# Optimization experiments

Hardware: AMD Instinct MI355X
Metric: run time of the kernel (lower is better)

## Reference

```python
import jax, jax.numpy as jnp
import numpy as np
from jax import lax

N, D, E = 20000, 1024, 320000
H, DH, M, ITERS, KC = 8, 64, 256, 6, 33   # nystrom heads, head dim, landmarks, pinv iters, res conv kernel
WQK, WATT, NC = 256, 128, 2               # custom-attn dim, MIL attn dim, n_classes


def _pinv(x, iters):
    # Moore-Penrose iterative pseudo-inverse (lucidrains nystrom-attention)
    ax = jnp.abs(x)
    z = jnp.swapaxes(x, -1, -2) / (ax.sum(-1).max() * ax.sum(-2).max())
    I = jnp.eye(x.shape[-1], dtype=x.dtype)
    for _ in range(iters):
        xz = x @ z
        z = 0.25 * z @ (13. * I - xz @ (15. * I - xz @ (7. * I - xz)))
    return z


def _nystrom(x, qkv_w, out_w, out_b, res_w):
    b, n, d = x.shape
    pad = (M - n % M) % M
    xp = jnp.pad(x, ((0, 0), (pad, 0), (0, 0)))  # pad at front, as in torch impl
    npd = n + pad
    q, k, v = jnp.split(xp @ qkv_w, 3, axis=-1)
    heads = lambda t: t.reshape(b, npd, H, DH).transpose(0, 2, 1, 3)  # [b,h,n,dh]
    q = heads(q) * (DH ** -0.5); k = heads(k); v = heads(v)
    l = npd // M
    ql = q.reshape(b, H, M, l, DH).sum(3) / l   # landmark means
    kl = k.reshape(b, H, M, l, DH).sum(3) / l
    a1 = jax.nn.softmax(jnp.einsum('bhid,bhjd->bhij', q, kl), -1)   # [b,h,n,m]
    a2 = jax.nn.softmax(jnp.einsum('bhid,bhjd->bhij', ql, kl), -1)  # [b,h,m,m]
    a3 = jax.nn.softmax(jnp.einsum('bhid,bhjd->bhij', ql, k), -1)   # [b,h,m,n]
    out = (a1 @ _pinv(a2, ITERS)) @ (a3 @ v)
    # depthwise residual conv along the sequence dim, per head
    res = lax.conv_general_dilated(v, res_w, (1, 1), ((KC // 2, KC // 2), (0, 0)),
                                   dimension_numbers=('NCHW', 'OIHW', 'NCHW'),
                                   feature_group_count=H)
    out = (out + res).transpose(0, 2, 1, 3).reshape(b, npd, H * DH)
    return (out @ out_w + out_b)[:, -n:]


def _forward(bag, adj_vals, qkv_w, out_w, out_b, res_w, wq_w, wq_b, wk_w, wk_b,
             wv_w, wv_b, va_w, va_b, ua_w, ua_b, wa_w, wa_b, fc_w, fc_b, fc_b2,
             adj_rows, adj_cols):
    enc = _nystrom(bag, qkv_w, out_w, out_b, res_w)        # [1,N,D]
    encoder_output = enc[0] + bag                           # xg + dense -> [1,N,D]
    # CustomAttention: per-edge q.k over sparse adjacency indices
    q = encoder_output[0] @ wq_w + wq_b                     # [N,256]
    k = encoder_output[0] @ wk_w + wk_b
    e = jnp.sum(q[adj_rows] * k[adj_cols], -1) / (WQK ** 0.5)
    # NeighborAggregator: sparse elementwise mul with adj then row-sum
    A_raw = jax.ops.segment_sum(e * adj_vals, adj_rows, num_segments=N)
    alpha = jax.nn.softmax(A_raw)                           # [N]
    value = bag @ wv_w + wv_b                               # [1,N,D]
    xl = alpha[:, None] * value                             # [1,N,D]
    sw = jax.nn.sigmoid(-xl) ** 2
    xo = xl * 2. * sw + 2. * encoder_output * (1. - sw)     # [1,N,D]
    # gated MIL attention (softmax over dim 0 of [1,N,1], as in source)
    inst = jnp.tanh(xo @ va_w + va_b) * jax.nn.sigmoid(xo @ ua_w + ua_b)
    k_alpha = jax.nn.softmax(inst @ wa_w + wa_b, axis=0)    # [1,N,1]
    pooled = (k_alpha * xo)[0].mean(0, keepdims=True)       # mean pooling -> [1,D]
    out = pooled @ fc_w + fc_b + fc_b2                      # [1,NC]
    return out, A_raw, k_alpha


def setup_inputs() -> dict:
    key = jax.random.key(0)
    ks = jax.random.split(key, 20)
    s = 0.02
    p = lambda k, shape: jax.random.normal(k, shape, jnp.float32) * s
    z = lambda n: jnp.zeros((n,), jnp.float32)
    return {
        'bag': jax.random.normal(ks[0], (1, N, D), jnp.float32),
        'adj_vals': jnp.ones((E,), jnp.float32),
        'qkv_w': p(ks[1], (D, 3 * H * DH)),
        'out_w': p(ks[2], (H * DH, D)), 'out_b': z(D),
        'res_w': p(ks[3], (H, 1, KC, 1)),
        'wq_w': p(ks[4], (D, WQK)), 'wq_b': z(WQK),
        'wk_w': p(ks[5], (D, WQK)), 'wk_b': z(WQK),
        'wv_w': p(ks[6], (D, D)), 'wv_b': z(D),
        'va_w': p(ks[7], (D, WATT)), 'va_b': z(WATT),
        'ua_w': p(ks[8], (D, WATT)), 'ua_b': z(WATT),
        'wa_w': p(ks[9], (WATT, 1)), 'wa_b': z(1),
        'fc_w': p(ks[10], (D, NC)), 'fc_b': z(NC), 'fc_b2': z(NC),
        'adj_rows': jax.random.randint(ks[11], (E,), 0, N),
        'adj_cols': jax.random.randint(ks[12], (E,), 0, N),
    }


def reference(bag, adj_vals, qkv_w, out_w, out_b, res_w, wq_w, wq_b, wk_w, wk_b,
              wv_w, wv_b, va_w, va_b, ua_w, ua_b, wa_w, wa_b, fc_w, fc_b, fc_b2,
              adj_rows, adj_cols):
    return _forward(bag, adj_vals, qkv_w, out_w, out_b, res_w, wq_w, wq_b, wk_w, wk_b,
                    wv_w, wv_b, va_w, va_b, ua_w, ua_b, wa_w, wa_b, fc_w, fc_b, fc_b2,
                    adj_rows, adj_cols)
```

## Files before the change

### kernel.cpp

```cpp
#include <hip/hip_runtime.h>
#include <math.h>

constexpr int NTOK = 20000;
constexpr int DIM  = 1024;
constexpr int NEDGE= 320000;
constexpr int NH   = 8;
constexpr int DH   = 64;
constexpr int NLM  = 256;
constexpr int PADF = 224;
constexpr int NPD  = 20224;
constexpr int LGRP = 79;
constexpr int PITERS = 6;
constexpr int JSPL = 16;
constexpr int JLEN = NPD / JSPL;
constexpr int NCHK = 79;

typedef unsigned short u16;
typedef _Float16 f16x8 __attribute__((ext_vector_type(8)));
typedef float    f32x4 __attribute__((ext_vector_type(4)));
typedef u16      u16x8 __attribute__((ext_vector_type(8)));
typedef u16      u16x4 __attribute__((ext_vector_type(4)));

__device__ __forceinline__ float warpSum(float v){
  #pragma unroll
  for (int o = 32; o; o >>= 1) v += __shfl_xor(v, o);
  return v;
}
__device__ __forceinline__ float warpMax(float v){
  #pragma unroll
  for (int o = 32; o; o >>= 1) v = fmaxf(v, __shfl_xor(v, o));
  return v;
}
__device__ __forceinline__ u16 f2h(float x){
  _Float16 h = (_Float16)x; return __builtin_bit_cast(u16, h);
}
__device__ __forceinline__ float h2f(u16 u){
  return (float)__builtin_bit_cast(_Float16, u);
}
__device__ __forceinline__ int swz3(int r){ return (r ^ (r >> 2)) & 3; }

__global__ void zero_kernel(float* __restrict__ p, int n)
{
  int i = blockIdx.x * 256 + threadIdx.x;
  if (i < n) p[i] = 0.f;
}

__global__ __launch_bounds__(256) void tsplit_kernel(
    const float* __restrict__ W, u16* __restrict__ Th, u16* __restrict__ Tl,
    int Kd, int Nd)
{
  __shared__ float tile[32][33];
  const int t = threadIdx.x, bx = blockIdx.x, by = blockIdx.y;
  {
    int kk = t >> 3, n4 = (t & 7) * 4;
    float4 v = *(const float4*)&W[(size_t)(by*32 + kk) * Nd + bx*32 + n4];
    tile[kk][n4+0] = v.x; tile[kk][n4+1] = v.y;
    tile[kk][n4+2] = v.z; tile[kk][n4+3] = v.w;
  }
  __syncthreads();
  int nn = t >> 3, k4 = (t & 7) * 4;
  u16x4 hv, lv;
  #pragma unroll
  for (int c = 0; c < 4; ++c) {
    float x = tile[k4 + c][nn];
    u16 h = f2h(x);
    hv[c] = h;
    lv[c] = f2h(x - h2f(h));
  }
  size_t o = (size_t)(bx*32 + nn) * Kd + by*32 + k4;
  *(u16x4*)&Th[o] = hv;
  *(u16x4*)&Tl[o] = lv;
}

__global__ __launch_bounds__(256) void gemm_h2_kernel(
    const float* __restrict__ A, int ashift, int arows,
    const u16* __restrict__ BTh, const u16* __restrict__ BTl,
    const float* __restrict__ bias, const float* __restrict__ add,
    float* __restrict__ C,
    float* __restrict__ Qd, float* __restrict__ Kd2, float* __restrict__ Vd,
    int M, int N, int Kdim)
{
  __shared__ __align__(16) u16 AsH[128*32];
  __shared__ __align__(16) u16 AsL[128*32];
  __shared__ __align__(16) u16 BsH[128*32];
  __shared__ __align__(16) u16 BsL[128*32];
  const int tid = threadIdx.x, lane = tid & 63, wv = tid >> 6;
  const int wr = wv >> 1, wc = wv & 1;
  const int bm = blockIdx.y * 128, bn = blockIdx.x * 128;

  const int rowA = tid >> 1, half = tid & 1;
  const int rg = bm + rowA;
  const unsigned r_a = (unsigned)(rg - ashift);
  const bool av = r_a < (unsigned)arows;
  const float* Ap = A + (size_t)r_a * Kdim + half * 16;
  const u16* Bph = BTh + (size_t)(bn + rowA) * Kdim + half * 16;
  const u16* Bpl = BTl + (size_t)(bn + rowA) * Kdim + half * 16;
  const int swa = swz3(rowA);
  const int pg0 = (half*2) ^ swa, pg1 = (half*2 + 1) ^ swa;
  u16* wA_h0 = &AsH[rowA*32 + pg0*8]; u16* wA_h1 = &AsH[rowA*32 + pg1*8];
  u16* wA_l0 = &AsL[rowA*32 + pg0*8]; u16* wA_l1 = &AsL[rowA*32 + pg1*8];
  u16* wB_h0 = &BsH[rowA*32 + pg0*8]; u16* wB_h1 = &BsH[rowA*32 + pg1*8];
  u16* wB_l0 = &BsL[rowA*32 + pg0*8]; u16* wB_l1 = &BsL[rowA*32 + pg1*8];

  f32x4 acc[4][4];
  #pragma unroll
  for (int i = 0; i < 4; ++i)
    #pragma unroll
    for (int j = 0; j < 4; ++j) acc[i][j] = 0;

  const int lg = lane >> 4;
  const int l15 = lane & 15;

  for (int kt = 0; kt < Kdim; kt += 32) {
    float x[16];
    if (av) {
      float4 v0 = *(const float4*)(Ap + kt);
      float4 v1 = *(const float4*)(Ap + kt + 4);
      float4 v2 = *(const float4*)(Ap + kt + 8);
      float4 v3 = *(const float4*)(Ap + kt + 12);
      x[0]=v0.x; x[1]=v0.y; x[2]=v0.z; x[3]=v0.w;
      x[4]=v1.x; x[5]=v1.y; x[6]=v1.z; x[7]=v1.w;
      x[8]=v2.x; x[9]=v2.y; x[10]=v2.z; x[11]=v2.w;
      x[12]=v3.x; x[13]=v3.y; x[14]=v3.z; x[15]=v3.w;
    } else {
      #pragma unroll
      for (int e = 0; e < 16; ++e) x[e] = 0.f;
    }
    u16x8 ah0, ah1, al0, al1;
    #pragma unroll
    for (int e = 0; e < 8; ++e) {
      u16 h = f2h(x[e]);      ah0[e] = h; al0[e] = f2h(x[e]     - h2f(h));
      u16 h2 = f2h(x[8+e]);   ah1[e] = h2; al1[e] = f2h(x[8+e] - h2f(h2));
    }
    u16x8 bh0 = *(const u16x8*)(Bph + kt);
    u16x8 bh1 = *(const u16x8*)(Bph + kt + 8);
    u16x8 bl0 = *(const u16x8*)(Bpl + kt);
    u16x8 bl1 = *(const u16x8*)(Bpl + kt + 8);

    __syncthreads();
    *(u16x8*)wA_h0 = ah0; *(u16x8*)wA_h1 = ah1;
    *(u16x8*)wA_l0 = al0; *(u16x8*)wA_l1 = al1;
    *(u16x8*)wB_h0 = bh0; *(u16x8*)wB_h1 = bh1;
    *(u16x8*)wB_l0 = bl0; *(u16x8*)wB_l1 = bl1;
    __syncthreads();

    f16x8 bh[4], bl[4];
    #pragma unroll
    for (int j = 0; j < 4; ++j) {
      int lb = wc*64 + j*16 + l15;
      int offb = lb*32 + ((lg ^ swz3(lb)) * 8);
      bh[j] = __builtin_bit_cast(f16x8, *(const u16x8*)&BsH[offb]);
      bl[j] = __builtin_bit_cast(f16x8, *(const u16x8*)&BsL[offb]);
    }
    #pragma unroll
    for (int i = 0; i < 4; ++i) {
      int la = wr*64 + i*16 + l15;
      int offa = la*32 + ((lg ^ swz3(la)) * 8);
      f16x8 ah = __builtin_bit_cast(f16x8, *(const u16x8*)&AsH[offa]);
      f16x8 al = __builtin_bit_cast(f16x8, *(const u16x8*)&AsL[offa]);
      #pragma unroll
      for (int j = 0; j < 4; ++j) {
        acc[i][j] = __builtin_amdgcn_mfma_f32_16x16x32_f16(ah, bh[j], acc[i][j], 0, 0, 0);
        acc[i][j] = __builtin_amdgcn_mfma_f32_16x16x32_f16(ah, bl[j], acc[i][j], 0, 0, 0);
        acc[i][j] = __builtin_amdgcn_mfma_f32_16x16x32_f16(al, bh[j], acc[i][j], 0, 0, 0);
      }
    }
  }

  if (Qd) {
    #pragma unroll
    for (int i = 0; i < 4; ++i) {
      int row0 = bm + wr*64 + i*16 + (lane>>4)*4;
      #pragma unroll
      for (int j = 0; j < 4; ++j) {
        int col = bn + wc*64 + j*16 + l15;
        int which = col >> 9;
        float* dst = (which == 0) ? Qd : (which == 1) ? Kd2 : Vd;
        float sc = (which == 0) ? 0.125f : 1.f;
        int h = (col >> 6) & 7, dh = col & 63;
        #pragma unroll
        for (int r = 0; r < 4; ++r) {
          int gr = row0 + r;
          dst[((size_t)h * NPD + gr) * 64 + dh] = acc[i][j][r] * sc;
        }
      }
    }
  } else {
    #pragma unroll
    for (int i = 0; i < 4; ++i) {
      int row0 = bm + wr*64 + i*16 + (lane>>4)*4;
      #pragma unroll
      for (int j = 0; j < 4; ++j) {
        int col = bn + wc*64 + j*16 + l15;
        float bv = bias ? bias[col] : 0.f;
        #pragma unroll
        for (int r = 0; r < 4; ++r) {
          int gr = row0 + r;
          if (gr < M) {
            float v = acc[i][j][r] + bv;
            if (add) v += add[(size_t)gr * N + col];
            C[(size_t)gr * N + col] = v;
          }
        }
      }
    }
  }
}

__global__ __launch_bounds__(256) void bgemm64_kernel(
    const float* __restrict__ A, const float* __restrict__ B, float* __restrict__ C,
    int Msub, int Nsub, int Ksub, float dval, int useDiag, float scale)
{
  const int h = blockIdx.z;
  const float* Ah = A + (size_t)h * Msub * Ksub;
  const float* Bh = B + (size_t)h * Ksub * Nsub;
  float* Ch = C + (size_t)h * Msub * Nsub;
  __shared__ float As[16][68];
  __shared__ float Bs[16][64];
  const int tid = threadIdx.x, tx = tid & 15, ty = tid >> 4;
  const int bm = blockIdx.y * 64, bn = blockIdx.x * 64;
  float acc[4][4] = {};
  for (int k0 = 0; k0 < Ksub; k0 += 16) {
    float ra[4], rb[4];
    #pragma unroll
    for (int i = 0; i < 4; ++i) {
      int e = tid + 256 * i;
      ra[i] = Ah[(size_t)(bm + (e >> 4)) * Ksub + k0 + (e & 15)];
      int brow = k0 + (e >> 6), bcol = bn + (e & 63);
      float bv = Bh[(size_t)brow * Nsub + bcol];
      if (useDiag) bv = ((brow == bcol) ? dval : 0.f) - bv;
      rb[i] = bv;
    }
    __syncthreads();
    #pragma unroll
    for (int i = 0; i < 4; ++i) {
      int e = tid + 256 * i;
      As[e & 15][e >> 4] = ra[i];
      Bs[e >> 6][e & 63] = rb[i];
    }
    __syncthreads();
    #pragma unroll
    for (int k = 0; k < 16; ++k) {
      float4 a = *(const float4*)&As[k][ty*4];
      float4 b = *(const float4*)&Bs[k][tx*4];
      float avv[4] = {a.x,a.y,a.z,a.w};
      float bvv[4] = {b.x,b.y,b.z,b.w};
      #pragma unroll
      for (int i = 0; i < 4; ++i)
        #pragma unroll
        for (int j = 0; j < 4; ++j)
          acc[i][j] += avv[i] * bvv[j];
    }
    __syncthreads();
  }
  #pragma unroll
  for (int i = 0; i < 4; ++i) {
    float4 v = {acc[i][0]*scale, acc[i][1]*scale, acc[i][2]*scale, acc[i][3]*scale};
    *(float4*)&Ch[(size_t)(bm + ty*4 + i) * Nsub + bn + tx*4] = v;
  }
}

__global__ __launch_bounds__(64) void landmark_kernel(
    const float* __restrict__ src, float* __restrict__ dst)
{
  int m = blockIdx.x, h = blockIdx.y, d = threadIdx.x;
  const float* p = src + ((size_t)h * NPD + (size_t)m * LGRP) * 64 + d;
  float acc = 0.f;
  for (int j = 0; j < LGRP; ++j) acc += p[(size_t)j * 64];
  dst[((size_t)h * NLM + m) * 64 + d] = acc / (float)LGRP;
}

__global__ __launch_bounds__(256) void a2_kernel(
    const float* __restrict__ qlm, const float* __restrict__ klm, float* __restrict__ a2)
{
  int i = blockIdx.x, h = blockIdx.y, t = threadIdx.x;
  int w = t >> 6, lane = t & 63;
  __shared__ float qs[64];
  __shared__ float wr[4], wr2[4];
  if (t < 64) qs[t] = qlm[((size_t)h * NLM + i) * 64 + t];
  __syncthreads();
  const float* kr = klm + ((size_t)h * NLM + t) * 64;
  float s = 0.f;
  #pragma unroll
  for (int d2 = 0; d2 < 64; d2 += 4) {
    float4 kv = *(const float4*)(kr + d2);
    s += qs[d2]*kv.x + qs[d2+1]*kv.y + qs[d2+2]*kv.z + qs[d2+3]*kv.w;
  }
  float mx = warpMax(s);
  if (lane == 0) wr[w] = mx;
  __syncthreads();
  mx = fmaxf(fmaxf(wr[0], wr[1]), fmaxf(wr[2], wr[3]));
  float e = expf(s - mx);
  float sm = warpSum(e);
  if (lane == 0) wr2[w] = sm;
  __syncthreads();
  sm = wr2[0] + wr2[1] + wr2[2] + wr2[3];
  a2[((size_t)h * NLM + i) * NLM + t] = e / sm;
}

__global__ __launch_bounds__(256) void rowcolmax_kernel(
    const float* __restrict__ a2, float* __restrict__ scal)
{
  int h = blockIdx.x >> 1, mode = blockIdx.x & 1, t = threadIdx.x;
  int w = t >> 6, lane = t & 63;
  float sum = 0.f;
  if (mode == 0) {
    const float* p = a2 + ((size_t)h * NLM + t) * NLM;
    for (int j = 0; j < NLM; ++j) sum += p[j];
  } else {
    const float* p = a2 + (size_t)h * NLM * NLM + t;
    for (int i = 0; i < NLM; ++i) sum += p[(size_t)i * NLM];
  }
  float mx = warpMax(sum);
  __shared__ float wr[4];
  if (lane == 0) wr[w] = mx;
  __syncthreads();
  if (t == 0) {
    float m2 = fmaxf(fmaxf(wr[0], wr[1]), fmaxf(wr[2], wr[3]));
    atomicMax((int*)&scal[mode], __float_as_int(m2));
  }
}

__global__ __launch_bounds__(256) void initz_kernel(
    const float* __restrict__ a2, const float* __restrict__ scal, float* __restrict__ z)
{
  int i = blockIdx.x, h = blockIdx.y, t = threadIdx.x;
  float inv = 1.f / (scal[0] * scal[1]);
  z[((size_t)h * NLM + i) * NLM + t] = a2[((size_t)h * NLM + t) * NLM + i] * inv;
}

__global__ __launch_bounds__(256) void st_gemm_kernel(
    const float* __restrict__ K, const float* __restrict__ QLM,
    float* __restrict__ ST, int hbase)
{
  const int z = blockIdx.z, h = hbase + z;
  const float* A  = K   + (size_t)h * NPD * 64;
  const float* Bq = QLM + (size_t)h * NLM * 64;
  float* C = ST + (size_t)z * NPD * NLM;
  __shared__ float As[16][132];
  __shared__ float Bs[16][132];
  const int tid = threadIdx.x;
  const int tx = tid & 15, ty = tid >> 4;
  const int bm = blockIdx.y * 128, bn = blockIdx.x * 128;
  float acc[8][8] = {};
  for (int k0 = 0; k0 < 64; k0 += 16) {
    float ra[8], rb[8];
    #pragma unroll
    for (int i = 0; i < 8; ++i) {
      int e = tid + 256 * i;
      ra[i] = A[(size_t)(bm + (e >> 4)) * 64 + k0 + (e & 15)];
      rb[i] = Bq[(size_t)(bn + (e & 127)) * 64 + k0 + (e >> 7)];
    }
    __syncthreads();
    #pragma unroll
    for (int i = 0; i < 8; ++i) {
      int e = tid + 256 * i;
      As[e & 15][e >> 4]  = ra[i];
      Bs[e >> 7][e & 127] = rb[i];
    }
    __syncthreads();
    #pragma unroll
    for (int k = 0; k < 16; ++k) {
      float4 a0 = *(const float4*)&As[k][ty*4];
      float4 a1 = *(const float4*)&As[k][64 + ty*4];
      float4 b0 = *(const float4*)&Bs[k][tx*4];
      float4 b1 = *(const float4*)&Bs[k][64 + tx*4];
      float av[8] = {a0.x,a0.y,a0.z,a0.w,a1.x,a1.y,a1.z,a1.w};
      float bv[8] = {b0.x,b0.y,b0.z,b0.w,b1.x,b1.y,b1.z,b1.w};
      #pragma unroll
      for (int i = 0; i < 8; ++i)
        #pragma unroll
        for (int j = 0; j < 8; ++j)
          acc[i][j] += av[i] * bv[j];
    }
  }
  #pragma unroll
  for (int i = 0; i < 8; ++i) {
    int r = bm + ((i < 4) ? (ty*4 + i) : (64 + ty*4 + (i - 4)));
    #pragma unroll
    for (int jh = 0; jh < 2; ++jh) {
      int c0 = bn + jh*64 + tx*4;
      float4 v = {acc[i][jh*4+0], acc[i][jh*4+1], acc[i][jh*4+2], acc[i][jh*4+3]};
      *(float4*)&C[(size_t)r * NLM + c0] = v;
    }
  }
}

__global__ __launch_bounds__(256) void smax1_kernel(
    const float* __restrict__ ST, float* __restrict__ PMAX)
{
  int c = blockIdx.x, z = blockIdx.y, i = threadIdx.x;
  const float* p = ST + (size_t)z * NPD * NLM + (size_t)c * 256 * NLM + i;
  float mx = -INFINITY;
  #pragma unroll 8
  for (int jj = 0; jj < 256; ++jj) mx = fmaxf(mx, p[(size_t)jj * NLM]);
  PMAX[((size_t)z * NCHK + c) * NLM + i] = mx;
}

__global__ __launch_bounds__(256) void smax2_kernel(
    const float* __restrict__ PMAX, float* __restrict__ MXB, int hbase)
{
  int z = blockIdx.x, i = threadIdx.x;
  float mx = -INFINITY;
  for (int c = 0; c < NCHK; ++c)
    mx = fmaxf(mx, PMAX[((size_t)z * NCHK + c) * NLM + i]);
  MXB[(size_t)(hbase + z) * NLM + i] = mx;
}

__global__ __launch_bounds__(256) void pv_kernel(
    const float* __restrict__ ST, const float* __restrict__ V,
    const float* __restrict__ MXB, float* __restrict__ AVACC,
    float* __restrict__ LSACC, int hbase)
{
  const int z = blockIdx.z, h = hbase + z;
  const int i0 = blockIdx.y * 64;
  const int j0 = blockIdx.x * JLEN;
  const float* STh = ST + (size_t)z * NPD * NLM;
  const float* Vh  = V  + (size_t)h * NPD * 64;
  const int tid = threadIdx.x, tx = tid & 15, ty = tid >> 4;
  const int il = tid & 63;
  const float mloc = MXB[(size_t)h * NLM + i0 + il];
  __shared__ float As[16][68];
  __shared__ float Bs[16][64];
  __shared__ float S4[4][64];
  float acc[4][4] = {};
  float psum = 0.f;
  for (int k0 = 0; k0 < JLEN; k0 += 16) {
    float pa[4], pb[4];
    #pragma unroll
    for (int r = 0; r < 4; ++r) {
      int jj = (tid >> 6) + 4 * r;
      int j  = j0 + k0 + jj;
      pa[r] = expf(STh[(size_t)j * NLM + i0 + il] - mloc);
      pb[r] = Vh[(size_t)j * 64 + il];
      psum += pa[r];
    }
    __syncthreads();
    #pragma unroll
    for (int r = 0; r < 4; ++r) {
      int jj = (tid >> 6) + 4 * r;
      As[jj][il] = pa[r];
      Bs[jj][il] = pb[r];
    }
    __syncthreads();
    #pragma unroll
    for (int k = 0; k < 16; ++k) {
      float4 a = *(const float4*)&As[k][ty*4];
      float4 b = *(const float4*)&Bs[k][tx*4];
      float av[4] = {a.x,a.y,a.z,a.w};
      float bv[4] = {b.x,b.y,b.z,b.w};
      #pragma unroll
      for (int i = 0; i < 4; ++i)
        #pragma unroll
        for (int j = 0; j < 4; ++j)
          acc[i][j] += av[i] * bv[j];
    }
    __syncthreads();
  }
  S4[tid >> 6][il] = psum;
  __syncthreads();
  if (tid < 64)
    atomicAdd(&LSACC[(size_t)h * NLM + i0 + tid],
              S4[0][tid] + S4[1][tid] + S4[2][tid] + S4[3][tid]);
  #pragma unroll
  for (int i = 0; i < 4; ++i)
    #pragma unroll
    for (int d = 0; d < 4; ++d)
      atomicAdd(&AVACC[((size_t)h * NLM + i0 + ty*4 + i) * 64 + tx*4 + d], acc[i][d]);
}

__global__ __launch_bounds__(64) void avnorm_kernel(
    const float* __restrict__ AVACC, const float* __restrict__ LSACC,
    float* __restrict__ AV)
{
  int m = blockIdx.x, h = blockIdx.y, d = threadIdx.x;
  size_t idx = ((size_t)h * NLM + m) * 64 + d;
  AV[idx] = AVACC[idx] / LSACC[(size_t)h * NLM + m];
}

__global__ __launch_bounds__(256) void a1_fused_kernel(
    const float* __restrict__ Q, const float* __restrict__ klm,
    const float* __restrict__ W, float* __restrict__ O1)
{
  int h = blockIdx.y;
  int rb = blockIdx.x * 8;
  int t = threadIdx.x;
  int w = t >> 6, lane = t & 63;
  __shared__ float qs[8][64];
  __shared__ float ps[8][256];
  __shared__ float Wl[128 * 64];
  for (int e = t; e < 8 * 64; e += 256) {
    int r = e >> 6, d2 = e & 63;
    qs[r][d2] = Q[((size_t)h * NPD + PADF + rb + r) * 64 + d2];
  }
  __syncthreads();
  const float* kr = klm + ((size_t)h * NLM + t) * 64;
  float s[8] = {};
  #pragma unroll
  for (int d2 = 0; d2 < 64; d2 += 4) {
    float4 kv = *(const float4*)(kr + d2);
    #pragma unroll
    for (int r = 0; r < 8; ++r)
      s[r] += qs[r][d2]*kv.x + qs[r][d2+1]*kv.y + qs[r][d2+2]*kv.z + qs[r][d2+3]*kv.w;
  }
  #pragma unroll
  for (int r = 0; r < 8; ++r) ps[r][t] = s[r];
  __syncthreads();
  for (int r = w; r < 8; r += 4) {
    float v0 = ps[r][lane], v1 = ps[r][lane+64], v2 = ps[r][lane+128], v3 = ps[r][lane+192];
    float mx = warpMax(fmaxf(fmaxf(v0, v1), fmaxf(v2, v3)));
    float e0 = expf(v0-mx), e1 = expf(v1-mx), e2 = expf(v2-mx), e3 = expf(v3-mx);
    float inv = 1.f / warpSum(e0 + e1 + e2 + e3);
    ps[r][lane] = e0*inv; ps[r][lane+64] = e1*inv; ps[r][lane+128] = e2*inv; ps[r][lane+192] = e3*inv;
  }
  const float* Wh = W + (size_t)h * NLM * 64;
  int r0 = t >> 6, d = t & 63;
  float accA = 0.f, accB = 0.f;
  for (int half = 0; half < 2; ++half) {
    __syncthreads();
    for (int e = t; e < 2048; e += 256)
      ((float4*)Wl)[e] = ((const float4*)(Wh + (size_t)half * 8192))[e];
    __syncthreads();
    #pragma unroll 16
    for (int j = 0; j < 128; ++j) {
      float wv = Wl[j * 64 + d];
      accA += ps[r0][half*128 + j] * wv;
      accB += ps[r0 + 4][half*128 + j] * wv;
    }
  }
  O1[((size_t)rb + r0) * 512 + h*64 + d] = accA;
  O1[((size_t)rb + r0 + 4) * 512 + h*64 + d] = accB;
}

__global__ __launch_bounds__(512) void conv_res_kernel(
    const float* __restrict__ V, const float* __restrict__ rw, float* __restrict__ O1)
{
  int t = threadIdx.x;
  int h = t >> 6, d = t & 63;
  int i = PADF + blockIdx.x;
  __shared__ float wsm[264];
  if (t < 264) wsm[t] = rw[t];
  __syncthreads();
  const float* vp = V + ((size_t)h * NPD + i - 16) * 64 + d;
  float acc = 0.f;
  #pragma unroll
  for (int k = 0; k < 33; ++k) {
    int row = i - 16 + k;
    float vv = (row < NPD) ? vp[(size_t)k * 64] : 0.f;
    acc += wsm[h*33 + k] * vv;
  }
  O1[(size_t)blockIdx.x * 512 + t] += acc;
}

__global__ __launch_bounds__(256) void edge_kernel(
    const float* __restrict__ Q2, const float* __restrict__ K2,
    const int* __restrict__ rows, const int* __restrict__ cols,
    const float* __restrict__ vals, float* __restrict__ A_raw)
{
  int e = blockIdx.x * 4 + (threadIdx.x >> 6);
  int lane = threadIdx.x & 63;
  int r = rows[e], c = cols[e];
  float4 q = *(const float4*)&Q2[(size_t)r * 256 + lane * 4];
  float4 k = *(const float4*)&K2[(size_t)c * 256 + lane * 4];
  float s = q.x*k.x + q.y*k.y + q.z*k.z + q.w*k.w;
  s = warpSum(s);
  if (lane == 0) atomicAdd(&A_raw[r], s * 0.0625f * vals[e]);
}

__global__ __launch_bounds__(1024) void softmax_vec_kernel(
    const float* __restrict__ x, float* __restrict__ y)
{
  __shared__ float red[1024];
  int t = threadIdx.x;
  float mx = -INFINITY;
  for (int i = t; i < NTOK; i += 1024) mx = fmaxf(mx, x[i]);
  red[t] = mx; __syncthreads();
  for (int s = 512; s > 0; s >>= 1) { if (t < s) red[t] = fmaxf(red[t], red[t+s]); __syncthreads(); }
  mx = red[0]; __syncthreads();
  float sm = 0.f;
  for (int i = t; i < NTOK; i += 1024) sm += expf(x[i] - mx);
  red[t] = sm; __syncthreads();
  for (int s = 512; s > 0; s >>= 1) { if (t < s) red[t] += red[t+s]; __syncthreads(); }
  sm = red[0];
  float inv = 1.f / sm;
  for (int i = t; i < NTOK; i += 1024) y[i] = expf(x[i] - mx) * inv;
}

__global__ __launch_bounds__(256) void xo_kernel(
    const float* __restrict__ alpha, float* __restrict__ VAL, const float* __restrict__ EO)
{
  int row = blockIdx.x, t = threadIdx.x;
  float a = alpha[row];
  size_t base = (size_t)row * 1024 + t * 4;
  float4 v = *(const float4*)&VAL[base];
  float4 e = *(const float4*)&EO[base];
  float xv[4] = {v.x, v.y, v.z, v.w};
  float ev[4] = {e.x, e.y, e.z, e.w};
  float xo[4];
  #pragma unroll
  for (int i = 0; i < 4; ++i) {
    float xl = a * xv[i];
    float sg = 1.f / (1.f + expf(xl));
    float sw = sg * sg;
    xo[i] = xl * 2.f * sw + 2.f * ev[i] * (1.f - sw);
  }
  float4 r = {xo[0], xo[1], xo[2], xo[3]};
  *(float4*)&VAL[base] = r;
}

__global__ void ones_kernel(float* __restrict__ p, int n)
{
  int i = blockIdx.x * 256 + threadIdx.x;
  if (i < n) p[i] = 1.f;
}

__global__ __launch_bounds__(256) void pooled_kernel(
    const float* __restrict__ XO, float* __restrict__ pool)
{
  int c = blockIdx.x * 256 + threadIdx.x;
  int r0 = blockIdx.y * 500;
  float acc = 0.f;
  for (int r = r0; r < r0 + 500; ++r) acc += XO[(size_t)r * DIM + c];
  atomicAdd(&pool[c], acc);
}

__global__ __launch_bounds__(128) void final_kernel(
    const float* __restrict__ pool, const float* __restrict__ fcw,
    const float* __restrict__ fcb, const float* __restrict__ fcb2,
    float* __restrict__ out)
{
  int t = threadIdx.x, c = t >> 6, lane = t & 63;
  float acc = 0.f;
  for (int d = lane; d < DIM; d += 64)
    acc += pool[d] * (1.f / (float)NTOK) * fcw[d * 2 + c];
  acc = warpSum(acc);
  if (lane == 0) out[c] = acc + fcb[c] + fcb2[c];
}

extern "C" void kernel_launch(void* const* d_in, const int* in_sizes, int n_in,
                              void* d_out, int out_size, void* d_ws, size_t ws_size,
                              hipStream_t stream)
{
  float* out = (float*)d_out;

  constexpr size_t QKV_SZ = (size_t)NH * NPD * DH;
  constexpr size_t O1_SZ  = (size_t)NTOK * 512;
  constexpr size_t EO_SZ  = (size_t)NTOK * DIM;
  float* w = (float*)d_ws;
  size_t o = 0;
  auto alloc = [&](size_t n) { float* p = w + o; o += (n + 3) & ~(size_t)3; return p; };
  float* Q    = alloc(QKV_SZ);
  float* K    = alloc(QKV_SZ);
  float* V    = alloc(QKV_SZ);
  float* O1   = alloc(O1_SZ);
  float* EO   = alloc(EO_SZ);
  float* QLM  = alloc((size_t)NH * NLM * DH);
  float* KLM  = alloc((size_t)NH * NLM * DH);
  float* A2   = alloc((size_t)NH * NLM * NLM);
  float* Z0   = alloc((size_t)NH * NLM * NLM);
  float* Z1   = alloc((size_t)NH * NLM * NLM);
  float* T1   = alloc((size_t)NH * NLM * NLM);
  float* T2   = alloc((size_t)NH * NLM * NLM);
  float* T3   = alloc((size_t)NH * NLM * NLM);
  float* AV   = alloc((size_t)NH * NLM * DH);
  float* WM   = alloc((size_t)NH * NLM * DH);
  float* ALPHA= alloc(NTOK);
  float* POOL = alloc(1024);
  float* SCAL = alloc(8);
  float* PMAX = alloc((size_t)4 * NCHK * NLM);
  float* MXB  = alloc((size_t)NH * NLM);
  float* AVACC= alloc((size_t)NH * NLM * DH);
  float* LSACC= alloc((size_t)NH * NLM);
  const size_t needed_bytes = o * sizeof(float);

  float* ST  = O1;
  float* VAL = V;
  float* Q2  = Q;
  float* K2  = K;
  u16* qkvT_h = (u16*)A2;
  u16* qkvT_l = qkvT_h + (size_t)1536 * 1024;
  u16* outT_h = (u16*)T1;
  u16* outT_l = outT_h + (size_t)1024 * 512;
  u16* wqT_h  = (u16*)T2;
  u16* wqT_l  = wqT_h + (size_t)256 * 1024;
  u16* wkT_h  = wqT_l + (size_t)256 * 1024;
  u16* wkT_l  = wkT_h + (size_t)256 * 1024;
  u16* wvT_h  = (u16*)Z0;
  u16* wvT_l  = (u16*)Z1;

  if (n_in < 23 || ws_size < needed_bytes || out_size < 2 + NTOK + NTOK) {
    int grid = out_size > 0 ? (out_size + 255) / 256 : 1;
    zero_kernel<<<grid, 256, 0, stream>>>(out, out_size);
    return;
  }

  const float* bag  = (const float*)d_in[0];
  const float* adjv = (const float*)d_in[1];
  const float* qkvw = (const float*)d_in[2];
  const float* outw = (const float*)d_in[3];
  const float* outb = (const float*)d_in[4];
  const float* resw = (const float*)d_in[5];
  const float* wqw  = (const float*)d_in[6];
  const float* wqb  = (const float*)d_in[7];
  const float* wkw  = (const float*)d_in[8];
  const float* wkb  = (const float*)d_in[9];
  const float* wvw  = (const float*)d_in[10];
  const float* wvb  = (const float*)d_in[11];
  const float* fcw  = (const float*)d_in[18];
  const float* fcb  = (const float*)d_in[19];
  const float* fcb2 = (const float*)d_in[20];
  const int* arows  = (const int*)d_in[21];
  const int* acols  = (const int*)d_in[22];

  float* A_raw  = out + 2;
  float* kalpha = A_raw + NTOK;

  zero_kernel<<<(NTOK + 255) / 256, 256, 0, stream>>>(A_raw, NTOK);
  zero_kernel<<<4, 256, 0, stream>>>(POOL, 1024);
  zero_kernel<<<1, 256, 0, stream>>>(SCAL, 8);
  zero_kernel<<<(131072 + 255) / 256, 256, 0, stream>>>(AVACC, 131072);
  zero_kernel<<<8, 256, 0, stream>>>(LSACC, 2048);

  tsplit_kernel<<<dim3(1536/32, 1024/32), 256, 0, stream>>>(qkvw, qkvT_h, qkvT_l, 1024, 1536);
  gemm_h2_kernel<<<dim3(1536/128, NPD/128), 256, 0, stream>>>(
      bag, PADF, NTOK, qkvT_h, qkvT_l, nullptr, nullptr, nullptr, Q, K, V, NPD, 1536, 1024);
  landmark_kernel<<<dim3(NLM, NH), 64, 0, stream>>>(Q, QLM);
  landmark_kernel<<<dim3(NLM, NH), 64, 0, stream>>>(K, KLM);
  a2_kernel<<<dim3(NLM, NH), 256, 0, stream>>>(QLM, KLM, A2);
  rowcolmax_kernel<<<16, 256, 0, stream>>>(A2, SCAL);
  initz_kernel<<<dim3(NLM, NH), 256, 0, stream>>>(A2, SCAL, Z0);

  auto bgemm = [&](const float* Ab, const float* Bb, float* Cb,
                   int Ms, int Ns, int Ks, float dval, int useDiag, float scale) {
    bgemm64_kernel<<<dim3(Ns/64, Ms/64, NH), 256, 0, stream>>>(Ab, Bb, Cb, Ms, Ns, Ks, dval, useDiag, scale);
  };
  float* zc = Z0; float* zn = Z1;
  for (int it = 0; it < PITERS; ++it) {
    bgemm(A2, zc, T1, NLM, NLM, NLM, 0.f,  0, 1.f);
    bgemm(T1, T1, T2, NLM, NLM, NLM, 7.f,  1, 1.f);
    bgemm(T1, T2, T3, NLM, NLM, NLM, 15.f, 1, 1.f);
    bgemm(zc, T3, zn, NLM, NLM, NLM, 13.f, 1, 0.25f);
    float* tmp = zc; zc = zn; zn = tmp;
  }

  for (int hb = 0; hb < NH; hb += 4) {
    st_gemm_kernel<<<dim3(NLM/128, NPD/128, 4), 256, 0, stream>>>(K, QLM, ST, hb);
    smax1_kernel<<<dim3(NCHK, 4), 256, 0, stream>>>(ST, PMAX);
    smax2_kernel<<<4, 256, 0, stream>>>(PMAX, MXB, hb);
    pv_kernel<<<dim3(JSPL, NLM/64, 4), 256, 0, stream>>>(ST, V, MXB, AVACC, LSACC, hb);
  }
  avnorm_kernel<<<dim3(NLM, NH), 64, 0, stream>>>(AVACC, LSACC, AV);

  bgemm(zc, AV, WM, NLM, DH, NLM, 0.f, 0, 1.f);
  a1_fused_kernel<<<dim3(NTOK/8, NH), 256, 0, stream>>>(Q, KLM, WM, O1);
  conv_res_kernel<<<NTOK, 512, 0, stream>>>(V, resw, O1);

  tsplit_kernel<<<dim3(1024/32, 512/32), 256, 0, stream>>>(outw, outT_h, outT_l, 512, 1024);
  gemm_h2_kernel<<<dim3(1024/128, (NTOK+127)/128), 256, 0, stream>>>(
      O1, 0, NTOK, outT_h, outT_l, outb, bag, EO, nullptr, nullptr, nullptr, NTOK, 1024, 512);

  tsplit_kernel<<<dim3(256/32, 1024/32), 256, 0, stream>>>(wqw, wqT_h, wqT_l, 1024, 256);
  tsplit_kernel<<<dim3(256/32, 1024/32), 256, 0, stream>>>(wkw, wkT_h, wkT_l, 1024, 256);
  gemm_h2_kernel<<<dim3(256/128, (NTOK+127)/128), 256, 0, stream>>>(
      EO, 0, NTOK, wqT_h, wqT_l, wqb, nullptr, Q2, nullptr, nullptr, nullptr, NTOK, 256, 1024);
  gemm_h2_kernel<<<dim3(256/128, (NTOK+127)/128), 256, 0, stream>>>(
      EO, 0, NTOK, wkT_h, wkT_l, wkb, nullptr, K2, nullptr, nullptr, nullptr, NTOK, 256, 1024);
  edge_kernel<<<NEDGE/4, 256, 0, stream>>>(Q2, K2, arows, acols, adjv, A_raw);
  softmax_vec_kernel<<<1, 1024, 0, stream>>>(A_raw, ALPHA);

  tsplit_kernel<<<dim3(1024/32, 1024/32), 256, 0, stream>>>(wvw, wvT_h, wvT_l, 1024, 1024);
  gemm_h2_kernel<<<dim3(1024/128, (NTOK+127)/128), 256, 0, stream>>>(
      bag, 0, NTOK, wvT_h, wvT_l, wvb, nullptr, VAL, nullptr, nullptr, nullptr, NTOK, 1024, 1024);
  xo_kernel<<<NTOK, 256, 0, stream>>>(ALPHA, VAL, EO);
  ones_kernel<<<(NTOK+255)/256, 256, 0, stream>>>(kalpha, NTOK);
  pooled_kernel<<<dim3(4, 40), 256, 0, stream>>>(VAL, POOL);
  final_kernel<<<1, 128, 0, stream>>>(POOL, fcw, fcb, fcb2, out);
}
```

Before: 2.564 ms.

## Move a1 softmax and pinv-weighted product onto split-fp16 MFMA

Replaces the scalar FP32 a1_fused kernel with an MFMA kernel that computes Q·KLM^T, the row softmax, and the product with the precomputed W matrix. It uses hi/lo fp16 splitting with three MFMAs per tile to keep roughly FP32 accuracy. Helper kernels pre-split the landmark keys and a transposed W into hi/lo halves. Each block now handles 64 rows instead of 8. This removes the heavy CUDA-core FMA work and repeated W reloads, at the cost of large LDS use and some precision loss from the split approximation.

```diff
diff --git a/kernel.cpp b/kernel.cpp
--- a/kernel.cpp
+++ b/kernel.cpp
@@ -37,12 +37,45 @@
 __device__ __forceinline__ float h2f(u16 u){
   return (float)__builtin_bit_cast(_Float16, u);
 }
-__device__ __forceinline__ int swz3(int r){ return (r ^ (r >> 2)) & 3; }
 
 __global__ void zero_kernel(float* __restrict__ p, int n)
 {
   int i = blockIdx.x * 256 + threadIdx.x;
   if (i < n) p[i] = 0.f;
+}
+
+__global__ void split_kernel(const float* __restrict__ x,
+                             u16* __restrict__ hi, u16* __restrict__ lo, int n)
+{
+  int i = blockIdx.x * 256 + threadIdx.x;
+  if (i < n) {
+    float v = x[i];
+    u16 h = f2h(v);
+    hi[i] = h; lo[i] = f2h(v - h2f(h));
+  }
+}
+
+__global__ __launch_bounds__(256) void wsplit_kernel(
+    const float* __restrict__ W, u16* __restrict__ Th, u16* __restrict__ Tl)
+{
+  __shared__ float tile[64][65];
+  const int t = threadIdx.x, kc = blockIdx.x, h = blockIdx.y;
+  const float* Wh_ = W + (size_t)h * NLM * 64 + (size_t)kc * 64 * 64;
+  #pragma unroll
+  for (int i = 0; i < 16; ++i) {
+    int idx = t + 256 * i;
+    tile[idx >> 6][idx & 63] = Wh_[idx];
+  }
+  __syncthreads();
+  #pragma unroll
+  for (int i = 0; i < 16; ++i) {
+    int idx = t + 256 * i;
+    int dh = idx >> 6, kl2 = idx & 63;
+    float v = tile[kl2][dh];
+    u16 hh = f2h(v);
+    size_t o = (size_t)h * 16384 + (size_t)dh * 256 + kc * 64 + kl2;
+    Th[o] = hh; Tl[o] = f2h(v - h2f(hh));
+  }
 }
 
 __global__ __launch_bounds__(256) void tsplit_kernel(
@@ -95,6 +128,7 @@
   const float* Ap = A + (size_t)r_a * Kdim + half * 16;
   const u16* Bph = BTh + (size_t)(bn + rowA) * Kdim + half * 16;
   const u16* Bpl = BTl + (size_t)(bn + rowA) * Kdim + half * 16;
+  auto swz3 = [](int r){ return (r ^ (r >> 2)) & 3; };
   const int swa = swz3(rowA);
   const int pg0 = (half*2) ^ swa, pg1 = (half*2 + 1) ^ swa;
   u16* wA_h0 = &AsH[rowA*32 + pg0*8]; u16* wA_h1 = &AsH[rowA*32 + pg1*8];
@@ -204,6 +238,160 @@
         }
       }
     }
+  }
+}
+
+__global__ __launch_bounds__(256) void a1_mfma_kernel(
+    const float* __restrict__ Q,
+    const u16* __restrict__ KLMH, const u16* __restrict__ KLML,
+    const u16* __restrict__ WTGH, const u16* __restrict__ WTGL,
+    float* __restrict__ O1)
+{
+  const int h = blockIdx.y;
+  const int rb = blockIdx.x * 64;
+  const int tid = threadIdx.x, lane = tid & 63, wv = tid >> 6;
+  const int l15 = lane & 15, lg = lane >> 4;
+
+  __shared__ __align__(16) u16 pool[51200];
+  u16* KH = pool;
+  u16* KL = pool + 18432;
+  u16* QH = pool + 36864;
+  u16* QL = pool + 41472;
+  u16* WTH = pool;
+  u16* WTL = pool + 16896;
+  u16* PH  = pool + 33792;
+  u16* PL  = pool + 42496;
+
+  {
+    const u16* sh = KLMH + ((size_t)h * 256 + tid) * 64;
+    const u16* sl = KLML + ((size_t)h * 256 + tid) * 64;
+    u16* dsh = KH + tid * 72;
+    u16* dsl = KL + tid * 72;
+    #pragma unroll
+    for (int g = 0; g < 8; ++g) {
+      *(u16x8*)(dsh + g*8) = *(const u16x8*)(sh + g*8);
+      *(u16x8*)(dsl + g*8) = *(const u16x8*)(sl + g*8);
+    }
+  }
+  {
+    int row = tid >> 2, cb = (tid & 3) * 16;
+    int qr = rb + row; if (qr > NTOK - 1) qr = NTOK - 1;
+    const float* src = Q + ((size_t)h * NPD + PADF + qr) * 64 + cb;
+    u16* qh_ = QH + row * 72 + cb;
+    u16* ql_ = QL + row * 72 + cb;
+    #pragma unroll
+    for (int e = 0; e < 16; e += 4) {
+      float4 v = *(const float4*)(src + e);
+      float xs[4] = {v.x, v.y, v.z, v.w};
+      #pragma unroll
+      for (int c2 = 0; c2 < 4; ++c2) {
+        u16 hh = f2h(xs[c2]);
+        qh_[e + c2] = hh;
+        ql_[e + c2] = f2h(xs[c2] - h2f(hh));
+      }
+    }
+  }
+  __syncthreads();
+
+  f32x4 accs[16];
+  #pragma unroll
+  for (int i = 0; i < 16; ++i) accs[i] = 0;
+  const int qrow = wv * 16 + l15;
+  #pragma unroll
+  for (int ks = 0; ks < 2; ++ks) {
+    f16x8 bh = *(const f16x8*)(QH + qrow*72 + ks*32 + lg*8);
+    f16x8 bl = *(const f16x8*)(QL + qrow*72 + ks*32 + lg*8);
+    #pragma unroll
+    for (int i = 0; i < 16; ++i) {
+      const int m = i*16 + l15;
+      f16x8 ah = *(const f16x8*)(KH + m*72 + ks*32 + lg*8);
+      f16x8 al = *(const f16x8*)(KL + m*72 + ks*32 + lg*8);
+      accs[i] = __builtin_amdgcn_mfma_f32_16x16x32_f16(ah, bh, accs[i], 0, 0, 0);
+      accs[i] = __builtin_amdgcn_mfma_f32_16x16x32_f16(ah, bl, accs[i], 0, 0, 0);
+      accs[i] = __builtin_amdgcn_mfma_f32_16x16x32_f16(al, bh, accs[i], 0, 0, 0);
+    }
+  }
+
+  float mx = -INFINITY;
+  #pragma unroll
+  for (int i = 0; i < 16; ++i)
+    #pragma unroll
+    for (int r = 0; r < 4; ++r) mx = fmaxf(mx, accs[i][r]);
+  mx = fmaxf(mx, __shfl_xor(mx, 16));
+  mx = fmaxf(mx, __shfl_xor(mx, 32));
+  float sm = 0.f;
+  #pragma unroll
+  for (int i = 0; i < 16; ++i)
+    #pragma unroll
+    for (int r = 0; r < 4; ++r) {
+      float e = expf(accs[i][r] - mx);
+      accs[i][r] = e;
+      sm += e;
+    }
+  sm += __shfl_xor(sm, 16);
+  sm += __shfl_xor(sm, 32);
+  const float inv = 1.f / sm;
+
+  __syncthreads();
+
+  {
+    int dh = tid >> 2, qt = tid & 3;
+    const u16* sh = WTGH + (size_t)h * 16384 + (size_t)dh * 256 + qt * 64;
+    const u16* sl = WTGL + (size_t)h * 16384 + (size_t)dh * 256 + qt * 64;
+    u16* dsh = WTH + dh * 264 + qt * 64;
+    u16* dsl = WTL + dh * 264 + qt * 64;
+    #pragma unroll
+    for (int g = 0; g < 8; ++g) {
+      *(u16x8*)(dsh + g*8) = *(const u16x8*)(sh + g*8);
+      *(u16x8*)(dsl + g*8) = *(const u16x8*)(sl + g*8);
+    }
+  }
+
+  f32x4 acco[4];
+  #pragma unroll
+  for (int i = 0; i < 4; ++i) acco[i] = 0;
+  #pragma unroll
+  for (int kh = 0; kh < 2; ++kh) {
+    #pragma unroll
+    for (int ii = 0; ii < 8; ++ii) {
+      int i = kh * 8 + ii;
+      int klocal = ii * 16 + lg * 4;
+      u16x4 hv, lv;
+      #pragma unroll
+      for (int r = 0; r < 4; ++r) {
+        float v = accs[i][r];
+        u16 hh = f2h(v);
+        hv[r] = hh; lv[r] = f2h(v - h2f(hh));
+      }
+      *(u16x4*)(PH + qrow * 136 + klocal) = hv;
+      *(u16x4*)(PL + qrow * 136 + klocal) = lv;
+    }
+    __syncthreads();
+    #pragma unroll
+    for (int ks = 0; ks < 4; ++ks) {
+      f16x8 bh = *(const f16x8*)(PH + qrow*136 + ks*32 + lg*8);
+      f16x8 bl = *(const f16x8*)(PL + qrow*136 + ks*32 + lg*8);
+      #pragma unroll
+      for (int i2 = 0; i2 < 4; ++i2) {
+        int dh = i2 * 16 + l15;
+        int ko = kh*128 + ks*32 + lg*8;
+        f16x8 ah = *(const f16x8*)(WTH + dh*264 + ko);
+        f16x8 al = *(const f16x8*)(WTL + dh*264 + ko);
+        acco[i2] = __builtin_amdgcn_mfma_f32_16x16x32_f16(ah, bh, acco[i2], 0, 0, 0);
+        acco[i2] = __builtin_amdgcn_mfma_f32_16x16x32_f16(ah, bl, acco[i2], 0, 0, 0);
+        acco[i2] = __builtin_amdgcn_mfma_f32_16x16x32_f16(al, bh, acco[i2], 0, 0, 0);
+      }
+    }
+    __syncthreads();
+  }
+
+  const int grow = rb + qrow;
+  if (grow < NTOK) {
+    #pragma unroll
+    for (int i2 = 0; i2 < 4; ++i2)
+      #pragma unroll
+      for (int r = 0; r < 4; ++r)
+        O1[(size_t)grow * 512 + h*64 + i2*16 + lg*4 + r] = acco[i2][r] * inv;
   }
 }
 
@@ -476,60 +664,6 @@
   int m = blockIdx.x, h = blockIdx.y, d = threadIdx.x;
   size_t idx = ((size_t)h * NLM + m) * 64 + d;
   AV[idx] = AVACC[idx] / LSACC[(size_t)h * NLM + m];
-}
-
-__global__ __launch_bounds__(256) void a1_fused_kernel(
-    const float* __restrict__ Q, const float* __restrict__ klm,
-    const float* __restrict__ W, float* __restrict__ O1)
-{
-  int h = blockIdx.y;
-  int rb = blockIdx.x * 8;
-  int t = threadIdx.x;
-  int w = t >> 6, lane = t & 63;
-  __shared__ float qs[8][64];
-  __shared__ float ps[8][256];
-  __shared__ float Wl[128 * 64];
-  for (int e = t; e < 8 * 64; e += 256) {
-    int r = e >> 6, d2 = e & 63;
-    qs[r][d2] = Q[((size_t)h * NPD + PADF + rb + r) * 64 + d2];
-  }
-  __syncthreads();
-  const float* kr = klm + ((size_t)h * NLM + t) * 64;
-  float s[8] = {};
-  #pragma unroll
-  for (int d2 = 0; d2 < 64; d2 += 4) {
-    float4 kv = *(const float4*)(kr + d2);
-    #pragma unroll
-    for (int r = 0; r < 8; ++r)
-      s[r] += qs[r][d2]*kv.x + qs[r][d2+1]*kv.y + qs[r][d2+2]*kv.z + qs[r][d2+3]*kv.w;
-  }
-  #pragma unroll
-  for (int r = 0; r < 8; ++r) ps[r][t] = s[r];
-  __syncthreads();
-  for (int r = w; r < 8; r += 4) {
-    float v0 = ps[r][lane], v1 = ps[r][lane+64], v2 = ps[r][lane+128], v3 = ps[r][lane+192];
-    float mx = warpMax(fmaxf(fmaxf(v0, v1), fmaxf(v2, v3)));
-    float e0 = expf(v0-mx), e1 = expf(v1-mx), e2 = expf(v2-mx), e3 = expf(v3-mx);
-    float inv = 1.f / warpSum(e0 + e1 + e2 + e3);
-    ps[r][lane] = e0*inv; ps[r][lane+64] = e1*inv; ps[r][lane+128] = e2*inv; ps[r][lane+192] = e3*inv;
-  }
-  const float* Wh = W + (size_t)h * NLM * 64;
-  int r0 = t >> 6, d = t & 63;
-  float accA = 0.f, accB = 0.f;
-  for (int half = 0; half < 2; ++half) {
-    __syncthreads();
-    for (int e = t; e < 2048; e += 256)
-      ((float4*)Wl)[e] = ((const float4*)(Wh + (size_t)half * 8192))[e];
-    __syncthreads();
-    #pragma unroll 16
-    for (int j = 0; j < 128; ++j) {
-      float wv = Wl[j * 64 + d];
-      accA += ps[r0][half*128 + j] * wv;
-      accB += ps[r0 + 4][half*128 + j] * wv;
-    }
-  }
-  O1[((size_t)rb + r0) * 512 + h*64 + d] = accA;
-  O1[((size_t)rb + r0 + 4) * 512 + h*64 + d] = accB;
 }
 
 __global__ __launch_bounds__(512) void conv_res_kernel(
@@ -671,12 +805,16 @@
   float* MXB  = alloc((size_t)NH * NLM);
   float* AVACC= alloc((size_t)NH * NLM * DH);
   float* LSACC= alloc((size_t)NH * NLM);
+  float* KSPL = alloc(131072);
+  float* WSPL = alloc(131072);
   const size_t needed_bytes = o * sizeof(float);
 
   float* ST  = O1;
   float* VAL = V;
   float* Q2  = Q;
   float* K2  = K;
+  u16* KLMH = (u16*)KSPL; u16* KLML = KLMH + (size_t)NH * NLM * DH;
+  u16* WTGH = (u16*)WSPL; u16* WTGL = WTGH + (size_t)NH * DH * NLM;
   u16* qkvT_h = (u16*)A2;
   u16* qkvT_l = qkvT_h + (size_t)1536 * 1024;
   u16* outT_h = (u16*)T1;
@@ -726,6 +864,7 @@
       bag, PADF, NTOK, qkvT_h, qkvT_l, nullptr, nullptr, nullptr, Q, K, V, NPD, 1536, 1024);
   landmark_kernel<<<dim3(NLM, NH), 64, 0, stream>>>(Q, QLM);
   landmark_kernel<<<dim3(NLM, NH), 64, 0, stream>>>(K, KLM);
+  split_kernel<<<512, 256, 0, stream>>>(KLM, KLMH, KLML, NH * NLM * DH);
   a2_kernel<<<dim3(NLM, NH), 256, 0, stream>>>(QLM, KLM, A2);
   rowcolmax_kernel<<<16, 256, 0, stream>>>(A2, SCAL);
   initz_kernel<<<dim3(NLM, NH), 256, 0, stream>>>(A2, SCAL, Z0);
@@ -752,7 +891,9 @@
   avnorm_kernel<<<dim3(NLM, NH), 64, 0, stream>>>(AVACC, LSACC, AV);
 
   bgemm(zc, AV, WM, NLM, DH, NLM, 0.f, 0, 1.f);
-  a1_fused_kernel<<<dim3(NTOK/8, NH), 256, 0, stream>>>(Q, KLM, WM, O1);
+  wsplit_kernel<<<dim3(4, NH), 256, 0, stream>>>(WM, WTGH, WTGL);
+  a1_mfma_kernel<<<dim3((NTOK + 63) / 64, NH), 256, 0, stream>>>(
+      Q, KLMH, KLML, WTGH, WTGL, O1);
   conv_res_kernel<<<NTOK, 512, 0, stream>>>(V, resw, O1);
 
   tsplit_kernel<<<dim3(1024/32, 512/32), 256, 0, stream>>>(outw, outT_h, outT_l, 512, 1024);
```

Result: faster. 2.311 ms (-9.9%).
